# Kernel optimization log

Measured on AMD Instinct MI355X. Metric: run time of the kernel, lower is better.

The kernel has to match this reference:

```python
import jax, jax.numpy as jnp
import numpy as np

B, S, E = 1, 2048, 2048
H = 16            # num_q_heads
DN = 128          # qk_nope_head_dim
DR = 64           # qk_rope_head_dim
DV = 128          # v_head_dim
R = 512           # kv_lora_rank
QLR = 1536        # q_lora_rank
EPS = 1e-6
ROPE_BASE = 10000.0


def _rmsnorm(x, w):
    var = jnp.mean(jnp.square(x), axis=-1, keepdims=True)
    return x * jax.lax.rsqrt(var + EPS) * w


def _rope_cos_sin(seqlen):
    inv_freq = 1.0 / (ROPE_BASE ** (jnp.arange(0, DR, 2, dtype=jnp.float32) / DR))
    ang = jnp.arange(seqlen, dtype=jnp.float32)[:, None] * inv_freq[None, :]  # [S, DR/2]
    cos = jnp.concatenate([jnp.cos(ang), jnp.cos(ang)], axis=-1)  # [S, DR]
    sin = jnp.concatenate([jnp.sin(ang), jnp.sin(ang)], axis=-1)
    return cos, sin


def _rotate_half(x):
    x1, x2 = jnp.split(x, 2, axis=-1)
    return jnp.concatenate([-x2, x1], axis=-1)


def setup_inputs() -> dict:
    key = jax.random.key(0)
    ks = jax.random.split(key, 8)
    sd = lambda fan_in: 1.0 / np.sqrt(fan_in)
    return {
        "x": jax.random.normal(ks[0], (B, S, E), jnp.float32),
        "w_q_a": jax.random.normal(ks[1], (E, QLR), jnp.float32) * sd(E),
        "q_a_ln_w": jnp.ones((QLR,), jnp.float32),
        "w_q_b": jax.random.normal(ks[2], (QLR, H * (DN + DR)), jnp.float32) * sd(QLR),
        "w_kv_a": jax.random.normal(ks[3], (E, R + DR), jnp.float32) * sd(E),
        "kv_a_ln_w": jnp.ones((R,), jnp.float32),
        "w_kv_b": jax.random.normal(ks[4], (R, H * (DN + DV)), jnp.float32) * sd(R),
        "w_o": jax.random.normal(ks[5], (H * DV, E), jnp.float32) * sd(H * DV),
    }


def reference(x, w_q_a, q_a_ln_w, w_q_b, w_kv_a, kv_a_ln_w, w_kv_b, w_o):
    b, s, _ = x.shape
    # --- low-rank query projection: q_a -> RMSNorm -> q_b ---
    q_a = _rmsnorm(x @ w_q_a, q_a_ln_w)                      # [b,s,QLR]
    q = (q_a @ w_q_b).reshape(b, s, H, DN + DR)               # [b,s,H,192]
    q_nope, q_pe = q[..., :DN], q[..., DN:]
    # --- compressed KV projection (MQA, single KV head) ---
    ckv_kpe = x @ w_kv_a                                      # [b,s,R+DR]
    ckv = _rmsnorm(ckv_kpe[..., :R], kv_a_ln_w)               # [b,s,R]
    k_pe = ckv_kpe[..., R:].reshape(b, s, 1, DR)              # [b,s,1,DR]
    # --- partial RoPE on the rope sub-dims only ---
    cos, sin = _rope_cos_sin(s)
    cos, sin = cos[None, :, None, :], sin[None, :, None, :]
    q_pe = q_pe * cos + _rotate_half(q_pe) * sin
    k_pe = k_pe * cos + _rotate_half(k_pe) * sin
    # --- weight absorption: fold W_uk into q, W_uv @ W_o into output ---
    w_kv = w_kv_b.reshape(R, H, DN + DV)
    w_uk = w_kv[..., :DN]                                     # [R,H,DN]
    w_uv = w_kv[..., DN:]                                     # [R,H,DV]
    w_o3 = w_o.reshape(H, DV, E)
    w_o_abs = jnp.einsum('rhd,hde->hre', w_uv, w_o3)          # [H,R,E]
    q_abs = jnp.einsum('bshd,rhd->bshr', q_nope, w_uk)        # [b,s,H,R]
    # --- attention in compressed (ckv + rope) space ---
    q_full = jnp.concatenate([q_abs, q_pe], axis=-1)          # [b,s,H,R+DR]
    k_full = jnp.concatenate([ckv, k_pe[:, :, 0, :]], axis=-1)  # [b,s,R+DR]
    sm_scale = (DN + DR) ** -0.5
    scores = jnp.einsum('bqhd,bkd->bhqk', q_full, k_full) * sm_scale
    causal = jnp.tril(jnp.ones((s, s), dtype=bool))
    scores = jnp.where(causal[None, None], scores, jnp.finfo(scores.dtype).min)
    attn = jax.nn.softmax(scores, axis=-1)
    o_ckv = jnp.einsum('bhqk,bkr->bqhr', attn, ckv)           # [b,s,H,R]
    # --- absorbed output projection, summed over heads ---
    y = jnp.einsum('bqhr,hre->bqe', o_ckv, w_o_abs)           # [b,s,E]
    return y
```

## Files before the change

kernel.cpp:

```cpp
#include <hip/hip_runtime.h>
#include <math.h>


typedef unsigned short u16;
typedef unsigned int u32;
typedef __bf16 bf16x8 __attribute__((ext_vector_type(8)));
typedef float f32x4 __attribute__((ext_vector_type(4)));
typedef unsigned short u16x8 __attribute__((ext_vector_type(8)));

__device__ __forceinline__ u16 f2b(float f) {
  u32 u = __float_as_uint(f);
  u += 0x7FFFu + ((u >> 16) & 1u);
  return (u16)(u >> 16);
}
__device__ __forceinline__ float b2f(u16 v) {
  return __uint_as_float(((u32)v) << 16);
}

#define GLDS(g, l) __builtin_amdgcn_global_load_lds( \
    (const __attribute__((address_space(1))) u32*)(g), \
    (__attribute__((address_space(3))) u32*)(l), 16, 0, 0)

#define MFMA(a, b, c) __builtin_amdgcn_mfma_f32_16x16x32_bf16(a, b, c, 0, 0, 0)

template<int N>
__device__ __forceinline__ void vm_barrier() {
  __builtin_amdgcn_s_waitcnt(0xF70 | N);
  __builtin_amdgcn_s_barrier();
}

#define N_ITEMS_G 160
__device__ __forceinline__ int nkc_of(int qt) { return (((qt >> 1) + 1) + 3) >> 2; }

__device__ __forceinline__ float block_sum(float v, float* red) {
#pragma unroll
  for (int off = 32; off > 0; off >>= 1) v += __shfl_down(v, off);
  const int lane = threadIdx.x & 63, w = threadIdx.x >> 6;
  if (lane == 0) red[w] = v;
  __syncthreads();
  float r = red[0] + red[1] + red[2] + red[3];
  __syncthreads();
  return r;
}

template<int OUTK>
__global__ __launch_bounds__(256) void gemm_mfma(
    const u16* __restrict__ A, const u16* __restrict__ B, void* __restrict__ Cv,
    int K, int lda, int ldb, int ldc, long sA, long sB, long sC)
{
  __shared__ u16 At[3][4096];
  __shared__ u16 Bt[3][4096];
  const u16* Ab = A + (long)blockIdx.z * sA;
  const u16* Bb = B + (long)blockIdx.z * sB;
  const int tid = threadIdx.x;
  const int w = tid >> 6, lane = tid & 63;
  const int m0 = blockIdx.y * 128, n0 = blockIdx.x * 128;
  const int wm = (w >> 1) * 64, wn = (w & 1) * 64;
  const int fr = lane & 15, fq = lane >> 4;

  const int c0 = w * 2, c1 = w * 2 + 1;
  const int e0 = (c0 * 64 + lane) * 8, e1 = (c1 * 64 + lane) * 8;
  const int r0 = e0 >> 5, col0 = e0 & 31;
  const int r1 = e1 >> 5, col1 = e1 & 31;

  const int nk = K >> 5;
  auto issue = [&](int kc) {
    const int k0 = kc * 32;
    u16* at = At[kc % 3];
    u16* bt = Bt[kc % 3];
    GLDS(Ab + (long)(m0 + r0) * lda + k0 + col0, at + c0 * 512);
    GLDS(Bb + (long)(n0 + r0) * ldb + k0 + col0, bt + c0 * 512);
    GLDS(Ab + (long)(m0 + r1) * lda + k0 + col1, at + c1 * 512);
    GLDS(Bb + (long)(n0 + r1) * ldb + k0 + col1, bt + c1 * 512);
  };

  f32x4 acc[4][4] = {};
  issue(0);
  issue(1);
  vm_barrier<4>();
  for (int kc = 0; kc < nk; ++kc) {
    if (kc + 2 < nk) issue(kc + 2);
    const u16* at = At[kc % 3];
    const u16* bt = Bt[kc % 3];
    bf16x8 af[4], bfr[4];
#pragma unroll
    for (int i = 0; i < 4; ++i)
      af[i] = *(const bf16x8*)(at + (wm + i * 16 + fr) * 32 + fq * 8);
#pragma unroll
    for (int j = 0; j < 4; ++j)
      bfr[j] = *(const bf16x8*)(bt + (wn + j * 16 + fr) * 32 + fq * 8);
#pragma unroll
    for (int i = 0; i < 4; ++i)
#pragma unroll
      for (int j = 0; j < 4; ++j)
        acc[i][j] = MFMA(af[i], bfr[j], acc[i][j]);
    if (kc + 1 < nk) {
      if (kc + 2 < nk) vm_barrier<4>();
      else vm_barrier<0>();
    }
  }

  if (OUTK == 0) {
    float* C = (float*)Cv + (long)blockIdx.z * sC;
#pragma unroll
    for (int i = 0; i < 4; ++i)
#pragma unroll
      for (int j = 0; j < 4; ++j) {
        long base = (long)(m0 + wm + i * 16 + fq * 4) * ldc + (n0 + wn + j * 16 + fr);
#pragma unroll
        for (int r = 0; r < 4; ++r) C[base + (long)r * ldc] = acc[i][j][r];
      }
  } else if (OUTK == 1) {
    u16* C = (u16*)Cv + (long)blockIdx.z * sC;
#pragma unroll
    for (int i = 0; i < 4; ++i)
#pragma unroll
      for (int j = 0; j < 4; ++j) {
        long base = (long)(m0 + wm + i * 16 + fq * 4) * ldc + (n0 + wn + j * 16 + fr);
#pragma unroll
        for (int r = 0; r < 4; ++r) C[base + (long)r * ldc] = f2b(acc[i][j][r]);
      }
  } else {
    u16* C = (u16*)Cv + (long)blockIdx.z * sC;
#pragma unroll
    for (int i = 0; i < 4; ++i)
#pragma unroll
      for (int j = 0; j < 4; ++j) {
        ushort4 v = { f2b(acc[i][j][0]), f2b(acc[i][j][1]),
                      f2b(acc[i][j][2]), f2b(acc[i][j][3]) };
        *(ushort4*)(C + (long)(n0 + wn + j * 16 + fr) * ldc + (m0 + wm + i * 16 + fq * 4)) = v;
      }
  }
}

__global__ void init_ctr(u32* ctr) {
  if (threadIdx.x < 8) ctr[threadIdx.x] = 0;
}

__global__ __launch_bounds__(256, 2) void attn_partial(
    const u16* __restrict__ qfb,
    const u16* __restrict__ kfb,
    const u16* __restrict__ vallT,
    u32* __restrict__ ctr,
    u16* __restrict__ pO,
    float* __restrict__ pS)
{
  __shared__ u16 Ks[3 * 8192];
  __shared__ u16 Ps[4 * 2176];
  __shared__ u32 cur;

  const int tid = threadIdx.x;
  const int w = tid >> 6, lane = tid & 63;
  const int fr = lane & 15, fq = lane >> 4;
  const float scale = 0.07216878364870323f;
  const int grp = (int)(blockIdx.x & 7);
  u16* Psw = Ps + w * 2176;

  const int krow0 = (w * 2) * 16 + (lane >> 2);
  const int krow1 = (w * 2 + 1) * 16 + (lane >> 2);
  const int kg0 = (lane & 3) ^ (krow0 & 3);
  const int kg1 = (lane & 3) ^ (krow1 & 3);

  while (true) {
    if (tid == 0) cur = atomicAdd(&ctr[grp], 1u);
    __syncthreads();
    const u32 it = cur;
    if (it >= N_ITEMS_G) break;

    int rem = (int)it, qt = 31, kc = 0, hh = 0;
    for (int q = 31; q >= 0; --q) {
      int cnt = nkc_of(q) * 2;
      if (rem < cnt) { qt = q; kc = rem >> 1; hh = rem & 1; break; }
      rem -= cnt;
    }
    const int h = grp + hh * 8;
    const u32 gslot = (u32)grp * N_ITEMS_G + it;
    const int q0 = qt * 64;
    const int ktt = (qt >> 1) + 1;
    const int kt0 = kc * 4, kt1 = min(kt0 + 4, ktt);

    bf16x8 aq[18];
    {
      const u16* qp = qfb + (long)(q0 + w * 16 + fr) * 9216 + h * 576 + fq * 8;
#pragma unroll
      for (int d = 0; d < 18; ++d) aq[d] = *(const bf16x8*)(qp + d * 32);
    }

    float m_run[4], l_run[4];
#pragma unroll
    for (int r = 0; r < 4; ++r) { m_run[r] = -1e30f; l_run[r] = 0.f; }
    f32x4 Oacc[8] = {};
    const u16* vlane = vallT + (long)h * 262144 + (long)fr * 2048 + fq * 8;

    auto issueG = [&](int kt, int gk, int gb) {
      const int k0i = kt * 128;
      u16* buf = Ks + gb * 8192;
#pragma unroll
      for (int c = 0; c < 2; ++c) {
        const int d0 = (gk * 2 + c) * 32;
        u16* dst = buf + c * 4096;
        GLDS(kfb + (long)(k0i + krow0) * 576 + d0 + kg0 * 8, dst + (w * 2) * 512);
        GLDS(kfb + (long)(k0i + krow1) * 576 + d0 + kg1 * 8, dst + (w * 2 + 1) * 512);
      }
    };

    issueG(kt0, 0, 0);
    issueG(kt0, 1, 1);

    for (int kt = kt0; kt < kt1; ++kt) {
      const int k0 = kt * 128;
      vm_barrier<4>();

      f32x4 sc[8] = {};
#pragma unroll
      for (int g = 0; g < 9; ++g) {
        const int gg = g + 2;
        if (gg <= 8) issueG(kt, gg, gg % 3);
        else if (kt + 1 < kt1) issueG(kt + 1, gg - 9, gg % 3);
        const u16* kb0 = Ks + (g % 3) * 8192;
        __builtin_amdgcn_s_setprio(1);
#pragma unroll
        for (int c = 0; c < 2; ++c) {
          const int d = 2 * g + c;
          const u16* kb = kb0 + c * 4096;
#pragma unroll
          for (int j = 0; j < 8; ++j) {
            const int row = j * 16 + fr;
            bf16x8 b = *(const bf16x8*)(kb + row * 32 + ((fq ^ (row & 3)) * 8));
            sc[j] = MFMA(aq[d], b, sc[j]);
          }
        }
        __builtin_amdgcn_s_setprio(0);
        if (g < 8) vm_barrier<4>();
      }

      const u16* vk = vlane + k0;
      bf16x8 vA[4], vB[4];
#pragma unroll
      for (int q = 0; q < 4; ++q) {
        vA[q] = *(const bf16x8*)(vk + (long)q * 32768);
        vB[q] = *(const bf16x8*)(vk + (long)(q + 4) * 32768);
      }

      const bool diag = (kt == ktt - 1);
#pragma unroll
      for (int r = 0; r < 4; ++r) {
        float mx = m_run[r];
#pragma unroll
        for (int j = 0; j < 8; ++j) {
          float s = sc[j][r] * scale;
          if (diag) {
            const int row = q0 + w * 16 + fq * 4 + r;
            const int col = k0 + j * 16 + fr;
            if (col > row) s = -1e30f;
          }
          sc[j][r] = s;
          mx = fmaxf(mx, s);
        }
        mx = fmaxf(mx, __shfl_xor(mx, 1));
        mx = fmaxf(mx, __shfl_xor(mx, 2));
        mx = fmaxf(mx, __shfl_xor(mx, 4));
        mx = fmaxf(mx, __shfl_xor(mx, 8));
        const float alpha = __expf(m_run[r] - mx);
        m_run[r] = mx;
        float sum = 0.f;
#pragma unroll
        for (int j = 0; j < 8; ++j) {
          float p = __expf(sc[j][r] - mx);
          sc[j][r] = p;
          sum += p;
        }
        sum += __shfl_xor(sum, 1);
        sum += __shfl_xor(sum, 2);
        sum += __shfl_xor(sum, 4);
        sum += __shfl_xor(sum, 8);
        l_run[r] = l_run[r] * alpha + sum;
#pragma unroll
        for (int jv = 0; jv < 8; ++jv) Oacc[jv][r] *= alpha;
#pragma unroll
        for (int j = 0; j < 8; ++j)
          Psw[(fq * 4 + r) * 136 + j * 16 + fr] = f2b(sc[j][r]);
      }

#pragma unroll
      for (int ks = 0; ks < 4; ++ks) {
        bf16x8 ap = *(const bf16x8*)(Psw + fr * 136 + ks * 32 + fq * 8);
        __builtin_amdgcn_s_setprio(1);
#pragma unroll
        for (int q = 0; q < 4; ++q) Oacc[q] = MFMA(ap, vA[q], Oacc[q]);
        __builtin_amdgcn_s_setprio(0);
        if (ks < 3) {
#pragma unroll
          for (int q = 0; q < 4; ++q)
            vA[q] = *(const bf16x8*)(vk + (long)q * 32768 + (ks + 1) * 32);
        }
        __builtin_amdgcn_s_setprio(1);
#pragma unroll
        for (int q = 0; q < 4; ++q) Oacc[q + 4] = MFMA(ap, vB[q], Oacc[q + 4]);
        __builtin_amdgcn_s_setprio(0);
        if (ks < 3) {
#pragma unroll
          for (int q = 0; q < 4; ++q)
            vB[q] = *(const bf16x8*)(vk + (long)(q + 4) * 32768 + (ks + 1) * 32);
        }
      }
    }

    const long po = (long)gslot * 8192;
#pragma unroll
    for (int r = 0; r < 4; ++r) {
      const int lr = w * 16 + fq * 4 + r;
      if (fr == 0) {
        pS[((long)gslot * 64 + lr) * 2] = m_run[r];
        pS[((long)gslot * 64 + lr) * 2 + 1] = l_run[r];
      }
#pragma unroll
      for (int jv = 0; jv < 8; ++jv)
        pO[po + (long)lr * 128 + jv * 16 + fr] = f2b(Oacc[jv][r]);
    }
  }
}

__global__ __launch_bounds__(256) void attn_reduce(
    const u16* __restrict__ pO, const float* __restrict__ pS,
    u16* __restrict__ ovb)
{
  const int h = blockIdx.x, qt = blockIdx.y;
  const int g = h & 7, hh = h >> 3;
  const int ktt = (qt >> 1) + 1;
  const int nkc = (ktt + 3) >> 2;
  int base = g * N_ITEMS_G;
  for (int q = qt + 1; q < 32; ++q) base += nkc_of(q) * 2;
  const int tid = threadIdx.x;
  const int r = tid >> 2, cq = (tid & 3) * 32;

  float m[4], l[4], wgt[4];
  float M = -1e30f;
  for (int i = 0; i < nkc; ++i) {
    const long slot = base + i * 2 + hh;
    m[i] = pS[(slot * 64 + r) * 2];
    l[i] = pS[(slot * 64 + r) * 2 + 1];
    M = fmaxf(M, m[i]);
  }
  float L = 0.f;
  for (int i = 0; i < nkc; ++i) { wgt[i] = __expf(m[i] - M); L += l[i] * wgt[i]; }
  const float inv = 1.0f / L;

  u16* orow = ovb + (long)(qt * 64 + r) * 2048 + h * 128 + cq;
  for (int c8 = 0; c8 < 32; c8 += 8) {
    float acc[8] = {};
    for (int i = 0; i < nkc; ++i) {
      const long slot = base + i * 2 + hh;
      const u16x8 v = *(const u16x8*)(pO + (slot * 64 + r) * 128 + cq + c8);
#pragma unroll
      for (int e = 0; e < 8; ++e) acc[e] += b2f(v[e]) * wgt[i];
    }
    u16x8 o;
#pragma unroll
    for (int e = 0; e < 8; ++e) o[e] = f2b(acc[e] * inv);
    *(u16x8*)(orow + c8) = o;
  }
}

__global__ __launch_bounds__(256) void cast_bf16(const float* __restrict__ in,
                                                 u16* __restrict__ out, long n) {
  long i = ((long)blockIdx.x * 256 + threadIdx.x) * 4;
  if (i >= n) return;
  float4 v = *(const float4*)(in + i);
  ushort4 o = { f2b(v.x), f2b(v.y), f2b(v.z), f2b(v.w) };
  *(ushort4*)(out + i) = o;
}

__global__ __launch_bounds__(256) void transpose_cast(const float* __restrict__ in,
    u16* __restrict__ out, int ldi, int ldo, long sIn, long sOut) {
  in += (long)blockIdx.z * sIn;
  out += (long)blockIdx.z * sOut;
  __shared__ u16 t[32][33];
  const int i0 = blockIdx.y * 32, j0 = blockIdx.x * 32;
  const int tx = threadIdx.x & 31, ty = threadIdx.x >> 5;
  for (int r = ty; r < 32; r += 8)
    t[r][tx] = f2b(in[(long)(i0 + r) * ldi + j0 + tx]);
  __syncthreads();
  for (int r = ty; r < 32; r += 8)
    out[(long)(j0 + r) * ldo + i0 + tx] = t[tx][r];
}

__global__ __launch_bounds__(256) void rmsnorm_cast(const float* __restrict__ in,
    const float* __restrict__ w, u16* __restrict__ out, int n, int ldin) {
  __shared__ float red[4];
  const float* row = in + (long)blockIdx.x * ldin;
  u16* orow = out + (long)blockIdx.x * n;
  float ss = 0.f;
  for (int i = threadIdx.x; i < n; i += 256) { float v = row[i]; ss += v * v; }
  float tot = block_sum(ss, red);
  float inv = rsqrtf(tot / (float)n + 1e-6f);
  for (int i = threadIdx.x; i < n; i += 256) orow[i] = f2b(row[i] * inv * w[i]);
}

__global__ __launch_bounds__(256) void rope_table(float* tab) {
  int s = blockIdx.x * 8 + (threadIdx.x >> 5), j = threadIdx.x & 31;
  double freq = pow(10000.0, -(double)j / 32.0);
  double ang = (double)s * freq;
  tab[s * 64 + j] = (float)cos(ang);
  tab[s * 64 + 32 + j] = (float)sin(ang);
}

__global__ __launch_bounds__(256) void build_kfull(const float* __restrict__ ckv,
    const float* __restrict__ lnw, const float* __restrict__ tab, u16* __restrict__ kfb) {
  __shared__ float red[4];
  const int s = blockIdx.x;
  const float* row = ckv + (long)s * 2176;
  float ss = 0.f;
  for (int i = threadIdx.x; i < 512; i += 256) { float v = row[i]; ss += v * v; }
  float tot = block_sum(ss, red);
  float inv = rsqrtf(tot / 512.0f + 1e-6f);
  u16* orow = kfb + (long)s * 576;
  for (int i = threadIdx.x; i < 512; i += 256) orow[i] = f2b(row[i] * inv * lnw[i]);
  if (threadIdx.x < 64) {
    int i = threadIdx.x, j = i & 31;
    float c = tab[s * 64 + j], sn = tab[s * 64 + 32 + j];
    float xv = row[512 + i];
    float rot = (i < 32) ? -row[512 + i + 32] : row[512 + i - 32];
    orow[512 + i] = f2b(xv * c + rot * sn);
  }
}

__global__ __launch_bounds__(256) void rope_qpe(const u16* __restrict__ qb,
    const float* __restrict__ tab, u16* __restrict__ qfb) {
  const int s = blockIdx.x;
  const int h = threadIdx.x >> 4;
  const int i0 = (threadIdx.x & 15) * 4;
  const u16* src = qb + (long)s * 3072 + h * 192 + 128;
  u16* dst = qfb + (long)s * 9216 + h * 576 + 512;
#pragma unroll
  for (int k = 0; k < 4; ++k) {
    const int i = i0 + k, j = i & 31;
    float c = tab[s * 64 + j], sn = tab[s * 64 + 32 + j];
    float xv = b2f(src[i]);
    float rot = (i < 32) ? -b2f(src[i + 32]) : b2f(src[i - 32]);
    dst[i] = f2b(xv * c + rot * sn);
  }
}

extern "C" void kernel_launch(void* const* d_in, const int* in_sizes, int n_in,
                              void* d_out, int out_size, void* d_ws, size_t ws_size,
                              hipStream_t stream) {
  const float* x      = (const float*)d_in[0];
  const float* w_q_a  = (const float*)d_in[1];
  const float* q_ln   = (const float*)d_in[2];
  const float* w_q_b  = (const float*)d_in[3];
  const float* w_kv_a = (const float*)d_in[4];
  const float* kv_ln  = (const float*)d_in[5];
  const float* w_kv_b = (const float*)d_in[6];
  const float* w_o    = (const float*)d_in[7];
  float* out = (float*)d_out;

  char* p = (char*)d_ws;
  float* tab   = (float*)p;  p += 524288;
  u16* wkvbb   = (u16*)p;    p += 4194304;
  u16* wuvT    = (u16*)p;    p += 2097152;
  u16* woT     = (u16*)p;    p += 8388608;
  u16* qfb     = (u16*)p;    p += 37748736;
  u16* vallT   = (u16*)p;    p += 8388608;
  u16* kfb     = (u16*)p;    p += 2359296;
  u16* ovb     = (u16*)p;    p += 8388608;
  char* tb = p;
  u16* xb      = (u16*)tb;
  u16* wabT    = (u16*)(tb + 8388608);
  float* qac   = (float*)(tb + 17301504);
  u16* qab     = (u16*)(tb + 35127296);
  u16* wqbT    = (u16*)(tb + 41418752);
  u16* qb      = (u16*)(tb + 50855936);
  u16* pO      = (u16*)tb;
  float* pS    = (float*)(tb + 20971520);
  u32* ctr     = (u32*)(tb + 21626880);

  rope_table<<<dim3(256), 256, 0, stream>>>(tab);

  cast_bf16<<<4096, 256, 0, stream>>>(x, xb, 4194304);
  transpose_cast<<<dim3(48, 64), 256, 0, stream>>>(w_q_a, wabT, 1536, 2048, 0, 0);
  transpose_cast<<<dim3(18, 64), 256, 0, stream>>>(w_kv_a, wabT + 1536 * 2048, 576, 2048, 0, 0);
  transpose_cast<<<dim3(96, 48), 256, 0, stream>>>(w_q_b, wqbT, 3072, 1536, 0, 0);
  cast_bf16<<<2048, 256, 0, stream>>>(w_kv_b, wkvbb, 2097152);
  transpose_cast<<<dim3(4, 16, 16), 256, 0, stream>>>(w_kv_b + 128, wuvT, 4096, 512, 256, 65536);
  transpose_cast<<<dim3(64, 64), 256, 0, stream>>>(w_o, woT, 2048, 2048, 0, 0);

  gemm_mfma<0><<<dim3(17, 16), 256, 0, stream>>>(
      xb, wabT, qac, 2048, 2048, 2048, 2176, 0, 0, 0);
  rmsnorm_cast<<<2048, 256, 0, stream>>>(qac, q_ln, qab, 1536, 2176);
  build_kfull<<<2048, 256, 0, stream>>>(qac + 1536, kv_ln, tab, kfb);

  gemm_mfma<1><<<dim3(24, 16), 256, 0, stream>>>(
      qab, wqbT, qb, 1536, 1536, 1536, 3072, 0, 0, 0);

  gemm_mfma<1><<<dim3(4, 16, 16), 256, 0, stream>>>(
      qb, wkvbb, qfb, 128, 3072, 4096, 9216, 192, 256, 576);
  rope_qpe<<<dim3(2048), 256, 0, stream>>>(qb, tab, qfb);

  gemm_mfma<2><<<dim3(1, 16, 16), 256, 0, stream>>>(
      kfb, wuvT, vallT, 512, 576, 512, 2048, 0, 65536, 262144);

  init_ctr<<<1, 64, 0, stream>>>(ctr);
  attn_partial<<<dim3(768), 256, 0, stream>>>(qfb, kfb, vallT, ctr, pO, pS);
  attn_reduce<<<dim3(16, 32), 256, 0, stream>>>(pO, pS, ovb);

  gemm_mfma<0><<<dim3(16, 16), 256, 0, stream>>>(
      ovb, woT, out, 2048, 2048, 2048, 2048, 0, 0, 0);
}
```

Baseline: 499.0 us.

## Split-K the first and final GEMMs and fuse partial-sum reduction into norms

```diff
diff --git a/kernel.cpp b/kernel.cpp
--- a/kernel.cpp
+++ b/kernel.cpp
@@ -131,6 +131,16 @@
         *(ushort4*)(C + (long)(n0 + wn + j * 16 + fr) * ldc + (m0 + wm + i * 16 + fq * 4)) = v;
       }
   }
+}
+
+__global__ __launch_bounds__(256) void add_f32(const float* __restrict__ a,
+    const float* __restrict__ b, float* __restrict__ o, long n) {
+  long i = ((long)blockIdx.x * 256 + threadIdx.x) * 4;
+  if (i >= n) return;
+  float4 va = *(const float4*)(a + i);
+  float4 vb = *(const float4*)(b + i);
+  float4 vo = { va.x + vb.x, va.y + vb.y, va.z + vb.z, va.w + vb.w };
+  *(float4*)(o + i) = vo;
 }
 
 __global__ void init_ctr(u32* ctr) {
@@ -386,15 +396,28 @@
 }
 
 __global__ __launch_bounds__(256) void rmsnorm_cast(const float* __restrict__ in,
-    const float* __restrict__ w, u16* __restrict__ out, int n, int ldin) {
+    const float* __restrict__ w, u16* __restrict__ out, int n, int ldin,
+    const float* __restrict__ in2) {
   __shared__ float red[4];
   const float* row = in + (long)blockIdx.x * ldin;
+  const float* row2 = in2 ? in2 + (long)blockIdx.x * ldin : nullptr;
   u16* orow = out + (long)blockIdx.x * n;
   float ss = 0.f;
-  for (int i = threadIdx.x; i < n; i += 256) { float v = row[i]; ss += v * v; }
+  if (row2) {
+    for (int i = threadIdx.x; i < n; i += 256) {
+      float v = row[i] + row2[i]; ss += v * v;
+    }
+  } else {
+    for (int i = threadIdx.x; i < n; i += 256) { float v = row[i]; ss += v * v; }
+  }
   float tot = block_sum(ss, red);
   float inv = rsqrtf(tot / (float)n + 1e-6f);
-  for (int i = threadIdx.x; i < n; i += 256) orow[i] = f2b(row[i] * inv * w[i]);
+  if (row2) {
+    for (int i = threadIdx.x; i < n; i += 256)
+      orow[i] = f2b((row[i] + row2[i]) * inv * w[i]);
+  } else {
+    for (int i = threadIdx.x; i < n; i += 256) orow[i] = f2b(row[i] * inv * w[i]);
+  }
 }
 
 __global__ __launch_bounds__(256) void rope_table(float* tab) {
@@ -406,21 +429,37 @@
 }
 
 __global__ __launch_bounds__(256) void build_kfull(const float* __restrict__ ckv,
-    const float* __restrict__ lnw, const float* __restrict__ tab, u16* __restrict__ kfb) {
+    const float* __restrict__ lnw, const float* __restrict__ tab,
+    u16* __restrict__ kfb, const float* __restrict__ ckv2) {
   __shared__ float red[4];
   const int s = blockIdx.x;
   const float* row = ckv + (long)s * 2176;
+  const float* row2 = ckv2 ? ckv2 + (long)s * 2176 : nullptr;
   float ss = 0.f;
-  for (int i = threadIdx.x; i < 512; i += 256) { float v = row[i]; ss += v * v; }
+  if (row2) {
+    for (int i = threadIdx.x; i < 512; i += 256) {
+      float v = row[i] + row2[i]; ss += v * v;
+    }
+  } else {
+    for (int i = threadIdx.x; i < 512; i += 256) { float v = row[i]; ss += v * v; }
+  }
   float tot = block_sum(ss, red);
   float inv = rsqrtf(tot / 512.0f + 1e-6f);
   u16* orow = kfb + (long)s * 576;
-  for (int i = threadIdx.x; i < 512; i += 256) orow[i] = f2b(row[i] * inv * lnw[i]);
+  if (row2) {
+    for (int i = threadIdx.x; i < 512; i += 256)
+      orow[i] = f2b((row[i] + row2[i]) * inv * lnw[i]);
+  } else {
+    for (int i = threadIdx.x; i < 512; i += 256)
+      orow[i] = f2b(row[i] * inv * lnw[i]);
+  }
   if (threadIdx.x < 64) {
     int i = threadIdx.x, j = i & 31;
     float c = tab[s * 64 + j], sn = tab[s * 64 + 32 + j];
-    float xv = row[512 + i];
-    float rot = (i < 32) ? -row[512 + i + 32] : row[512 + i - 32];
+    float xv = row[512 + i] + (row2 ? row2[512 + i] : 0.f);
+    float rv = (i < 32) ? row[512 + i + 32] + (row2 ? row2[512 + i + 32] : 0.f)
+                        : row[512 + i - 32] + (row2 ? row2[512 + i - 32] : 0.f);
+    float rot = (i < 32) ? -rv : rv;
     orow[512 + i] = f2b(xv * c + rot * sn);
   }
 }
@@ -471,9 +510,13 @@
   u16* qab     = (u16*)(tb + 35127296);
   u16* wqbT    = (u16*)(tb + 41418752);
   u16* qb      = (u16*)(tb + 50855936);
+  float* qacB  = (float*)(tb + 63438848);
+  const size_t need_split1 = (size_t)(tb - (char*)d_ws) + 63438848 + 17825792;
+  const bool split1 = ws_size >= need_split1;
   u16* pO      = (u16*)tb;
   float* pS    = (float*)(tb + 20971520);
   u32* ctr     = (u32*)(tb + 21626880);
+  float* outP  = (float*)tb;
 
   rope_table<<<dim3(256), 256, 0, stream>>>(tab);
 
@@ -485,10 +528,17 @@
   transpose_cast<<<dim3(4, 16, 16), 256, 0, stream>>>(w_kv_b + 128, wuvT, 4096, 512, 256, 65536);
   transpose_cast<<<dim3(64, 64), 256, 0, stream>>>(w_o, woT, 2048, 2048, 0, 0);
 
-  gemm_mfma<0><<<dim3(17, 16), 256, 0, stream>>>(
-      xb, wabT, qac, 2048, 2048, 2048, 2176, 0, 0, 0);
-  rmsnorm_cast<<<2048, 256, 0, stream>>>(qac, q_ln, qab, 1536, 2176);
-  build_kfull<<<2048, 256, 0, stream>>>(qac + 1536, kv_ln, tab, kfb);
+  if (split1) {
+    gemm_mfma<0><<<dim3(17, 16, 2), 256, 0, stream>>>(
+        xb, wabT, qac, 1024, 2048, 2048, 2176, 1024, 1024, (long)(qacB - qac));
+  } else {
+    gemm_mfma<0><<<dim3(17, 16), 256, 0, stream>>>(
+        xb, wabT, qac, 2048, 2048, 2048, 2176, 0, 0, 0);
+  }
+  rmsnorm_cast<<<2048, 256, 0, stream>>>(qac, q_ln, qab, 1536, 2176,
+                                         split1 ? qacB : nullptr);
+  build_kfull<<<2048, 256, 0, stream>>>(qac + 1536, kv_ln, tab, kfb,
+                                        split1 ? qacB + 1536 : nullptr);
 
   gemm_mfma<1><<<dim3(24, 16), 256, 0, stream>>>(
       qab, wqbT, qb, 1536, 1536, 1536, 3072, 0, 0, 0);
@@ -501,9 +551,10 @@
       kfb, wuvT, vallT, 512, 576, 512, 2048, 0, 65536, 262144);
 
   init_ctr<<<1, 64, 0, stream>>>(ctr);
-  attn_partial<<<dim3(768), 256, 0, stream>>>(qfb, kfb, vallT, ctr, pO, pS);
+  attn_partial<<<dim3(512), 256, 0, stream>>>(qfb, kfb, vallT, ctr, pO, pS);
   attn_reduce<<<dim3(16, 32), 256, 0, stream>>>(pO, pS, ovb);
 
-  gemm_mfma<0><<<dim3(16, 16), 256, 0, stream>>>(
-      ovb, woT, out, 2048, 2048, 2048, 2048, 0, 0, 0);
-}
+  gemm_mfma<0><<<dim3(16, 16, 2), 256, 0, stream>>>(
+      ovb, woT, outP, 1024, 2048, 2048, 2048, 1024, 1024, 4194304);
+  add_f32<<<4096, 256, 0, stream>>>(outP, outP + 4194304, out, 4194304);
+}
```

After: 482.1 us. 3.4% less time.
